# Performance work log

Hardware: AMD Instinct MI355X
Metric: run time of the kernel (lower is better)

## Reference

```python
import math
import jax, jax.numpy as jnp
import numpy as np


def _pairwise_sqdist(x, y):
    # x: [N, d], y: [M, d] -> [N, M]
    x2 = jnp.sum(x * x, axis=-1)[:, None]
    y2 = jnp.sum(y * y, axis=-1)[None, :]
    return jnp.maximum(x2 + y2 - 2.0 * (x @ y.T), 0.0)


def setup_inputs() -> dict:
    key = jax.random.key(0)
    k1, k2 = jax.random.split(key)
    N, M, D = 8192, 8192, 2
    base_points = jax.random.normal(k1, (N, D), dtype=jnp.float32)
    target_points = jax.random.normal(k2, (M, D), dtype=jnp.float32)
    log_sigma = jnp.asarray(math.log(0.1), dtype=jnp.float32)
    log_scale = jnp.zeros((D,), dtype=jnp.float32)
    return {
        "base_points": base_points,
        "target_points": target_points,
        "log_sigma": log_sigma,
        "log_scale": log_scale,
    }


def reference(base_points, target_points, log_sigma, log_scale):
    # learn_scale=True: anisotropic per-coordinate scaling
    scale = jnp.exp(log_scale)
    base = base_points * scale
    target = target_points * scale

    # uniform node weights (use_weight_net=False)
    N = base.shape[0]
    M = target.shape[0]
    w_base = jnp.full((N,), 1.0 / N, dtype=base.dtype)
    w_target = jnp.full((M,), 1.0 / M, dtype=target.dtype)

    # center=True: subtract weighted centroid of each cloud
    base = base - jnp.sum(w_base[:, None] * base, axis=0, keepdims=True)
    target = target - jnp.sum(w_target[:, None] * target, axis=0, keepdims=True)

    sigma = jnp.exp(log_sigma)
    inv2s2 = 1.0 / (2.0 * sigma * sigma)

    k_bb = jnp.exp(-_pairwise_sqdist(base, base) * inv2s2)      # [N, N]
    k_tt = jnp.exp(-_pairwise_sqdist(target, target) * inv2s2)  # [M, M]
    k_bt = jnp.exp(-_pairwise_sqdist(base, target) * inv2s2)    # [N, M]

    term_bb = w_base @ (k_bb @ w_base)
    term_tt = w_target @ (k_tt @ w_target)
    term_bt = w_base @ (k_bt @ w_target)
    loss = term_bb + term_tt - 2.0 * term_bt
    return loss
```

## Files before the change

### kernel.cpp

```cpp
#include <hip/hip_runtime.h>


#define BLOCK 256
#define NT_CROSS 1024
#define NT_TOT   2080
#define LOG2E  1.4426950408889634f
#define NBUCK  512
#define BXMIN  (-64.0f)
#define BSCALE 4.0f
#define CUT    6.32455532f

typedef float v2f __attribute__((ext_vector_type(2)));

struct Prep { float f0, f1, sh0, sh1; };

__device__ __forceinline__ float fexp2(float x) {
    return __builtin_amdgcn_exp2f(x);
}

__global__ __launch_bounds__(1024) void prep_kernel(
    const float* __restrict__ base, const float* __restrict__ target,
    const float* __restrict__ log_sigma, const float* __restrict__ log_scale,
    int N, int M, Prep* __restrict__ pp, double* __restrict__ slots)
{
    __shared__ double mred[16][4];
    const int tid = threadIdx.x;
    if (tid < 64) slots[tid] = 0.0;

    double sbx = 0, sby = 0, stx = 0, sty = 0;
    const float4* b4 = (const float4*)base;
    const float4* t4 = (const float4*)target;
    for (int i = tid; i < (N >> 1); i += 1024) {
        float4 v = b4[i];
        sbx += (double)v.x + (double)v.z;
        sby += (double)v.y + (double)v.w;
    }
    for (int i = tid; i < (M >> 1); i += 1024) {
        float4 v = t4[i];
        stx += (double)v.x + (double)v.z;
        sty += (double)v.y + (double)v.w;
    }
    for (int off = 32; off; off >>= 1) {
        sbx += __shfl_down(sbx, off); sby += __shfl_down(sby, off);
        stx += __shfl_down(stx, off); sty += __shfl_down(sty, off);
    }
    if ((tid & 63) == 0) {
        mred[tid >> 6][0] = sbx; mred[tid >> 6][1] = sby;
        mred[tid >> 6][2] = stx; mred[tid >> 6][3] = sty;
    }
    __syncthreads();
    if (tid == 0) {
        double b0 = 0, b1 = 0, t0 = 0, t1 = 0;
        for (int k = 0; k < 16; ++k) {
            b0 += mred[k][0]; b1 += mred[k][1];
            t0 += mred[k][2]; t1 += mred[k][3];
        }
        float s0 = expf(log_scale[0]);
        float s1 = expf(log_scale[1]);
        float sigma = expf(log_sigma[0]);
        float inv2s2 = 1.0f / (2.0f * sigma * sigma);
        float sq = sqrtf(inv2s2 * LOG2E);
        float f0 = s0 * sq, f1 = s1 * sq;
        pp->f0 = f0; pp->f1 = f1;
        pp->sh0 = (float)(b0 / (double)N - t0 / (double)M) * f0;
        pp->sh1 = (float)(b1 / (double)N - t1 / (double)M) * f1;
    }
}

__global__ __launch_bounds__(1024) void sort_kernel(
    const float* __restrict__ base, const float* __restrict__ target,
    int N, int M, const Prep* __restrict__ pp,
    float* __restrict__ xsB, float* __restrict__ ysB, float* __restrict__ csB,
    float* __restrict__ xsT, float* __restrict__ ysT, float* __restrict__ csT)
{
    __shared__ unsigned hist[NBUCK];
    __shared__ unsigned pref[NBUCK];
    __shared__ unsigned cnt[NBUCK];
    const int tid = threadIdx.x;
    const Prep p = *pp;
    const bool isB = (blockIdx.x == 0);
    const float2* src = (const float2*)(isB ? base : target);
    const int n = isB ? N : M;
    float* xs = isB ? xsB : xsT;
    float* ys = isB ? ysB : ysT;
    float* cs = isB ? csB : csT;
    const float shx = isB ? p.sh0 : 0.f;
    const float shy = isB ? p.sh1 : 0.f;

    for (int i = tid; i < NBUCK; i += 1024) { hist[i] = 0u; cnt[i] = 0u; }
    __syncthreads();
    for (int i = tid; i < n; i += 1024) {
        float2 a = src[i];
        float x = fmaf(a.x, p.f0, -shx);
        int b = (int)((x - BXMIN) * BSCALE);
        b = min(max(b, 0), NBUCK - 1);
        atomicAdd(&hist[b], 1u);
    }
    __syncthreads();
    if (tid < NBUCK) pref[tid] = hist[tid];
    __syncthreads();
    for (int off = 1; off < NBUCK; off <<= 1) {
        unsigned v = 0u;
        if (tid < NBUCK && tid >= off) v = pref[tid - off];
        __syncthreads();
        if (tid < NBUCK) pref[tid] += v;
        __syncthreads();
    }
    for (int i = tid; i < n; i += 1024) {
        float2 a = src[i];
        float x = fmaf(a.x, p.f0, -shx);
        float y = fmaf(a.y, p.f1, -shy);
        int b = (int)((x - BXMIN) * BSCALE);
        b = min(max(b, 0), NBUCK - 1);
        unsigned pos = pref[b] - hist[b] + atomicAdd(&cnt[b], 1u);
        xs[pos] = x;
        ys[pos] = y;
        cs[pos] = -fmaf(x, x, y * y);
    }
}

__global__ __launch_bounds__(BLOCK, 8) void mmd_main(
    int N, int M,
    const float* __restrict__ xsB, const float* __restrict__ ysB,
    const float* __restrict__ csB,
    const float* __restrict__ xsT, const float* __restrict__ ysT,
    const float* __restrict__ csT,
    double* __restrict__ slots)
{
    __shared__ __align__(16) float tbx[256];
    __shared__ __align__(16) float tby[256];
    __shared__ __align__(16) float tbc[256];
    __shared__ __align__(8)  float2 qb[64];
    __shared__ double wredd[4];

    const int tid = threadIdx.x;
    const int t   = (int)(((long long)blockIdx.x * 997) % NT_TOT);

    const double wNN = 1.0 / ((double)N * (double)N);
    const double wMM = 1.0 / ((double)M * (double)M);
    const double wNM = -2.0 / ((double)N * (double)M);

    int ib, jb, term;
    bool diag;
    const float* xA; const float* yA; const float* cA;
    const float* xB; const float* yB; const float* cB;
    double wt;
    if (t < NT_CROSS) {
        ib = t >> 5; jb = t & 31;
        xA = xsB; yA = ysB; cA = csB;
        xB = xsT; yB = ysT; cB = csT;
        wt = wNM; diag = false; term = 2;
    } else {
        const int u = t - NT_CROSS;
        term = (u >= 528) ? 1 : 0;
        const int v = u - term * 528;
        int r = (int)((65.0f - sqrtf(4225.0f - 8.0f * (float)v)) * 0.5f);
        r = min(max(r, 0), 31);
        while (r > 0 && (r * (65 - r)) / 2 > v) --r;
        while (r < 31 && ((r + 1) * (64 - r)) / 2 <= v) ++r;
        ib = r;
        jb = r + (v - (r * (65 - r)) / 2);
        diag = (jb == ib);
        if (term) { xA = xsT; yA = ysT; cA = csT; }
        else      { xA = xsB; yA = ysB; cA = csB; }
        xB = xA; yB = yA; cB = cA;
        wt = 2.0 * (term ? wMM : wNN);
    }
    const int i0 = ib * 256, j0 = jb * 256;

    tbx[tid] = xB[j0 + tid];
    tby[tid] = yB[j0 + tid];
    tbc[tid] = cB[j0 + tid];
    if (tid < 64) {
        float4 q4 = ((const float4*)(xB + j0))[tid];
        float qlo = fminf(fminf(q4.x, q4.y), fminf(q4.z, q4.w));
        float qhi = fmaxf(fmaxf(q4.x, q4.y), fmaxf(q4.z, q4.w));
        qb[tid] = make_float2(qlo, qhi);
    }
    __syncthreads();

    const int u_  = tid & 127;
    const int r0  = i0 + 2 * u_;
    const int js  = (tid >> 7) * 128;

    float2 xr = ((const float2*)xA)[r0 >> 1];
    float2 yr = ((const float2*)yA)[r0 >> 1];
    float2 cr = ((const float2*)cA)[r0 >> 1];
    float ax2s[2] = { xr.x + xr.x, xr.y + xr.y };
    float ay2s[2] = { yr.x + yr.x, yr.y + yr.y };
    float A0s[2]  = { cr.x, cr.y };

    float rmin = fminf(xr.x, xr.y);
    float rmax = fmaxf(xr.x, xr.y);
    for (int off = 32; off; off >>= 1) {
        rmin = fminf(rmin, __shfl_xor(rmin, off));
        rmax = fmaxf(rmax, __shfl_xor(rmax, off));
    }
    const float rminc = rmin - CUT;
    const float rmaxc = rmax + CUT;

    const float4* bx4 = (const float4*)(tbx + js);
    const float4* by4 = (const float4*)(tby + js);
    const float4* c4  = (const float4*)(tbc + js);
    const int qoff = js >> 2;

    double result;
    if (!diag) {
        v2f s00 = {0.f, 0.f}, s01 = {0.f, 0.f};
        v2f s10 = {0.f, 0.f}, s11 = {0.f, 0.f};
#pragma unroll 2
        for (int q = 0; q < 32; ++q) {
            float2 qr = qb[qoff + q];
            if (qr.x > rmaxc || qr.y < rminc) continue;
            float4 BX = bx4[q];
            float4 BY = by4[q];
            float4 C  = c4[q];
            v2f bxa = { BX.x, BX.y }, bxb = { BX.z, BX.w };
            v2f bya = { BY.x, BY.y }, byb = { BY.z, BY.w };
            v2f ca  = { C.x,  C.y  }, cb  = { C.z,  C.w  };
            {
                v2f A0v = { A0s[0], A0s[0] };
                v2f axv = { ax2s[0], ax2s[0] };
                v2f ayv = { ay2s[0], ay2s[0] };
                v2f ea = axv * bxa + (ayv * bya + (ca + A0v));
                v2f eb = axv * bxb + (ayv * byb + (cb + A0v));
                s00 += (v2f){ fexp2(ea.x), fexp2(ea.y) };
                s01 += (v2f){ fexp2(eb.x), fexp2(eb.y) };
            }
            {
                v2f A0v = { A0s[1], A0s[1] };
                v2f axv = { ax2s[1], ax2s[1] };
                v2f ayv = { ay2s[1], ay2s[1] };
                v2f ea = axv * bxa + (ayv * bya + (ca + A0v));
                v2f eb = axv * bxb + (ayv * byb + (cb + A0v));
                s10 += (v2f){ fexp2(ea.x), fexp2(ea.y) };
                s11 += (v2f){ fexp2(eb.x), fexp2(eb.y) };
            }
        }
        v2f st0 = s00 + s01;
        v2f st1 = s10 + s11;
        result = wt * ((double)(st0.x + st0.y) + (double)(st1.x + st1.y));
    } else {
        float sge = 0.f, sgt = 0.f;
        const int jbase = j0 + js;
#pragma unroll 2
        for (int q = 0; q < 32; ++q) {
            float2 qr = qb[qoff + q];
            if (qr.x > rmaxc || qr.y < rminc) continue;
            float4 BX = bx4[q];
            float4 BY = by4[q];
            float4 C  = c4[q];
            const int j = jbase + 4 * q;
#pragma unroll
            for (int k = 0; k < 2; ++k) {
                const int row = r0 + k;
                float e0 = fmaf(ax2s[k], BX.x, fmaf(ay2s[k], BY.x, C.x + A0s[k]));
                float e1 = fmaf(ax2s[k], BX.y, fmaf(ay2s[k], BY.y, C.y + A0s[k]));
                float e2 = fmaf(ax2s[k], BX.z, fmaf(ay2s[k], BY.z, C.z + A0s[k]));
                float e3 = fmaf(ax2s[k], BX.w, fmaf(ay2s[k], BY.w, C.w + A0s[k]));
                float v0 = fexp2(e0), v1 = fexp2(e1);
                float v2 = fexp2(e2), v3 = fexp2(e3);
                sge += (j + 0 >= row) ? v0 : 0.f;  sgt += (j + 0 > row) ? v0 : 0.f;
                sge += (j + 1 >= row) ? v1 : 0.f;  sgt += (j + 1 > row) ? v1 : 0.f;
                sge += (j + 2 >= row) ? v2 : 0.f;  sgt += (j + 2 > row) ? v2 : 0.f;
                sge += (j + 3 >= row) ? v3 : 0.f;  sgt += (j + 3 > row) ? v3 : 0.f;
            }
        }
        result = (term ? wMM : wNN) * (double)(sge + sgt);
    }

    for (int off = 32; off; off >>= 1) result += __shfl_down(result, off);
    if ((tid & 63) == 0) wredd[tid >> 6] = result;
    __syncthreads();
    if (tid == 0) {
        double s = wredd[0] + wredd[1] + wredd[2] + wredd[3];
        atomicAdd(&slots[blockIdx.x & 63], s);
    }
}

__global__ void final_kernel(const double* __restrict__ slots,
                             float* __restrict__ out)
{
    const int tid = threadIdx.x;
    double s = slots[tid];
    for (int off = 32; off; off >>= 1) s += __shfl_down(s, off);
    if (tid == 0) out[0] = (float)s;
}

extern "C" void kernel_launch(void* const* d_in, const int* in_sizes, int n_in,
                              void* d_out, int out_size, void* d_ws, size_t ws_size,
                              hipStream_t stream)
{
    const float* base      = (const float*)d_in[0];
    const float* target    = (const float*)d_in[1];
    const float* log_sigma = (const float*)d_in[2];
    const float* log_scale = (const float*)d_in[3];
    float* out = (float*)d_out;

    int N = in_sizes[0] / 2;
    int M = in_sizes[1] / 2;

    char* ws = (char*)d_ws;
    Prep*   pp    = (Prep*)ws;
    double* slots = (double*)(ws + 256);
    float*  arr   = (float*)(ws + 1024);
    float* xsB = arr;
    float* ysB = xsB + N;
    float* csB = ysB + N;
    float* xsT = csB + N;
    float* ysT = xsT + M;
    float* csT = ysT + M;

    prep_kernel<<<1, 1024, 0, stream>>>(base, target, log_sigma, log_scale,
                                        N, M, pp, slots);
    sort_kernel<<<2, 1024, 0, stream>>>(base, target, N, M, pp,
                                        xsB, ysB, csB, xsT, ysT, csT);
    mmd_main<<<NT_TOT, BLOCK, 0, stream>>>(N, M, xsB, ysB, csB,
                                           xsT, ysT, csT, slots);
    final_kernel<<<1, 64, 0, stream>>>(slots, out);
}
```

Baseline: 102.1 us.

## Fuse prep into sort and interleave column tiles for balanced MMD blocks

Removes the separate prep kernel. Each sort block now computes its own coordinate sums, and the base-minus-target centroid shift is applied per row inside the main kernel. Column tiles are now strided (phase-interleaved) rather than contiguous, so every block sees a spread of the sorted x-range, and the symmetric terms use full 32x32 grids with a per-block triangular mask instead of the upper-triangle enumeration. The cutoff radius is reduced. The goals are fewer launches and more even per-block work, at the cost of launching more blocks (3072) and losing some pruning locality from the interleaving.

```diff
diff --git a/kernel.cpp b/kernel.cpp
--- a/kernel.cpp
+++ b/kernel.cpp
@@ -1,102 +1,69 @@
 #include <hip/hip_runtime.h>
 
 
-#define BLOCK 256
+#define BLOCK    256
 #define NT_CROSS 1024
-#define NT_TOT   2080
-#define LOG2E  1.4426950408889634f
-#define NBUCK  512
-#define BXMIN  (-64.0f)
-#define BSCALE 4.0f
-#define CUT    6.32455532f
+#define NT_TOT   3072
+#define NBUCK    512
+#define BXMIN    (-64.0f)
+#define BSCALE   4.0f
+#define CUT      5.2915026f
+#define LOG2E    1.4426950408889634f
 
 typedef float v2f __attribute__((ext_vector_type(2)));
-
-struct Prep { float f0, f1, sh0, sh1; };
 
 __device__ __forceinline__ float fexp2(float x) {
     return __builtin_amdgcn_exp2f(x);
 }
 
-__global__ __launch_bounds__(1024) void prep_kernel(
+__global__ __launch_bounds__(1024) void sort_kernel(
     const float* __restrict__ base, const float* __restrict__ target,
     const float* __restrict__ log_sigma, const float* __restrict__ log_scale,
-    int N, int M, Prep* __restrict__ pp, double* __restrict__ slots)
+    int N, int M,
+    float* __restrict__ xsB, float* __restrict__ ysB, float* __restrict__ csB,
+    float* __restrict__ xsT, float* __restrict__ ysT, float* __restrict__ csT,
+    double* __restrict__ msum, double* __restrict__ slots)
 {
-    __shared__ double mred[16][4];
+    __shared__ unsigned hist[NBUCK], pref[NBUCK], cnt[NBUCK];
+    __shared__ double mred[16][2];
     const int tid = threadIdx.x;
-    if (tid < 64) slots[tid] = 0.0;
-
-    double sbx = 0, sby = 0, stx = 0, sty = 0;
-    const float4* b4 = (const float4*)base;
-    const float4* t4 = (const float4*)target;
-    for (int i = tid; i < (N >> 1); i += 1024) {
-        float4 v = b4[i];
-        sbx += (double)v.x + (double)v.z;
-        sby += (double)v.y + (double)v.w;
-    }
-    for (int i = tid; i < (M >> 1); i += 1024) {
-        float4 v = t4[i];
-        stx += (double)v.x + (double)v.z;
-        sty += (double)v.y + (double)v.w;
-    }
-    for (int off = 32; off; off >>= 1) {
-        sbx += __shfl_down(sbx, off); sby += __shfl_down(sby, off);
-        stx += __shfl_down(stx, off); sty += __shfl_down(sty, off);
-    }
-    if ((tid & 63) == 0) {
-        mred[tid >> 6][0] = sbx; mred[tid >> 6][1] = sby;
-        mred[tid >> 6][2] = stx; mred[tid >> 6][3] = sty;
-    }
-    __syncthreads();
-    if (tid == 0) {
-        double b0 = 0, b1 = 0, t0 = 0, t1 = 0;
-        for (int k = 0; k < 16; ++k) {
-            b0 += mred[k][0]; b1 += mred[k][1];
-            t0 += mred[k][2]; t1 += mred[k][3];
-        }
-        float s0 = expf(log_scale[0]);
-        float s1 = expf(log_scale[1]);
-        float sigma = expf(log_sigma[0]);
-        float inv2s2 = 1.0f / (2.0f * sigma * sigma);
-        float sq = sqrtf(inv2s2 * LOG2E);
-        float f0 = s0 * sq, f1 = s1 * sq;
-        pp->f0 = f0; pp->f1 = f1;
-        pp->sh0 = (float)(b0 / (double)N - t0 / (double)M) * f0;
-        pp->sh1 = (float)(b1 / (double)N - t1 / (double)M) * f1;
-    }
-}
-
-__global__ __launch_bounds__(1024) void sort_kernel(
-    const float* __restrict__ base, const float* __restrict__ target,
-    int N, int M, const Prep* __restrict__ pp,
-    float* __restrict__ xsB, float* __restrict__ ysB, float* __restrict__ csB,
-    float* __restrict__ xsT, float* __restrict__ ysT, float* __restrict__ csT)
-{
-    __shared__ unsigned hist[NBUCK];
-    __shared__ unsigned pref[NBUCK];
-    __shared__ unsigned cnt[NBUCK];
-    const int tid = threadIdx.x;
-    const Prep p = *pp;
     const bool isB = (blockIdx.x == 0);
+    if (isB && tid < 64) slots[tid] = 0.0;
+
+    const float sigma = expf(log_sigma[0]);
+    const float sq = sqrtf((0.5f / (sigma * sigma)) * LOG2E);
+    const float f0 = expf(log_scale[0]) * sq;
+    const float f1 = expf(log_scale[1]) * sq;
+
     const float2* src = (const float2*)(isB ? base : target);
     const int n = isB ? N : M;
     float* xs = isB ? xsB : xsT;
     float* ys = isB ? ysB : ysT;
     float* cs = isB ? csB : csT;
-    const float shx = isB ? p.sh0 : 0.f;
-    const float shy = isB ? p.sh1 : 0.f;
 
     for (int i = tid; i < NBUCK; i += 1024) { hist[i] = 0u; cnt[i] = 0u; }
     __syncthreads();
+
+    double sx = 0.0, sy = 0.0;
     for (int i = tid; i < n; i += 1024) {
         float2 a = src[i];
-        float x = fmaf(a.x, p.f0, -shx);
-        int b = (int)((x - BXMIN) * BSCALE);
-        b = min(max(b, 0), NBUCK - 1);
+        float x = a.x * f0, y = a.y * f1;
+        sx += (double)x; sy += (double)y;
+        int b = min(max((int)((x - BXMIN) * BSCALE), 0), NBUCK - 1);
         atomicAdd(&hist[b], 1u);
     }
-    __syncthreads();
+    for (int off = 32; off; off >>= 1) {
+        sx += __shfl_down(sx, off);
+        sy += __shfl_down(sy, off);
+    }
+    if ((tid & 63) == 0) { mred[tid >> 6][0] = sx; mred[tid >> 6][1] = sy; }
+    __syncthreads();
+    if (tid == 0) {
+        double ax = 0, ay = 0;
+        for (int k = 0; k < 16; ++k) { ax += mred[k][0]; ay += mred[k][1]; }
+        msum[2 * blockIdx.x] = ax; msum[2 * blockIdx.x + 1] = ay;
+    }
+
     if (tid < NBUCK) pref[tid] = hist[tid];
     __syncthreads();
     for (int off = 1; off < NBUCK; off <<= 1) {
@@ -108,10 +75,8 @@
     }
     for (int i = tid; i < n; i += 1024) {
         float2 a = src[i];
-        float x = fmaf(a.x, p.f0, -shx);
-        float y = fmaf(a.y, p.f1, -shy);
-        int b = (int)((x - BXMIN) * BSCALE);
-        b = min(max(b, 0), NBUCK - 1);
+        float x = a.x * f0, y = a.y * f1;
+        int b = min(max((int)((x - BXMIN) * BSCALE), 0), NBUCK - 1);
         unsigned pos = pref[b] - hist[b] + atomicAdd(&cnt[b], 1u);
         xs[pos] = x;
         ys[pos] = y;
@@ -125,7 +90,7 @@
     const float* __restrict__ csB,
     const float* __restrict__ xsT, const float* __restrict__ ysT,
     const float* __restrict__ csT,
-    double* __restrict__ slots)
+    const double* __restrict__ msum, double* __restrict__ slots)
 {
     __shared__ __align__(16) float tbx[256];
     __shared__ __align__(16) float tby[256];
@@ -134,87 +99,88 @@
     __shared__ double wredd[4];
 
     const int tid = threadIdx.x;
-    const int t   = (int)(((long long)blockIdx.x * 997) % NT_TOT);
+    const int t   = blockIdx.x;
 
     const double wNN = 1.0 / ((double)N * (double)N);
     const double wMM = 1.0 / ((double)M * (double)M);
     const double wNM = -2.0 / ((double)N * (double)M);
 
-    int ib, jb, term;
-    bool diag;
-    const float* xA; const float* yA; const float* cA;
-    const float* xB; const float* yB; const float* cB;
+    int rt, phase, term;
+    bool sym;
+    const float *xA, *yA, *xB, *yB, *cB;
     double wt;
+    float shx = 0.f, shy = 0.f;
     if (t < NT_CROSS) {
-        ib = t >> 5; jb = t & 31;
-        xA = xsB; yA = ysB; cA = csB;
-        xB = xsT; yB = ysT; cB = csT;
-        wt = wNM; diag = false; term = 2;
+        sym = false; term = 2;
+        rt = t >> 5; phase = t & 31;
+        xA = xsB; yA = ysB; xB = xsT; yB = ysT; cB = csT;
+        wt = wNM;
+        shx = (float)(msum[0] / (double)N - msum[2] / (double)M);
+        shy = (float)(msum[1] / (double)N - msum[3] / (double)M);
     } else {
+        sym = true;
         const int u = t - NT_CROSS;
-        term = (u >= 528) ? 1 : 0;
-        const int v = u - term * 528;
-        int r = (int)((65.0f - sqrtf(4225.0f - 8.0f * (float)v)) * 0.5f);
-        r = min(max(r, 0), 31);
-        while (r > 0 && (r * (65 - r)) / 2 > v) --r;
-        while (r < 31 && ((r + 1) * (64 - r)) / 2 <= v) ++r;
-        ib = r;
-        jb = r + (v - (r * (65 - r)) / 2);
-        diag = (jb == ib);
-        if (term) { xA = xsT; yA = ysT; cA = csT; }
-        else      { xA = xsB; yA = ysB; cA = csB; }
-        xB = xA; yB = yA; cB = cA;
+        term = (u >= 1024) ? 1 : 0;
+        const int v = u & 1023;
+        rt = v >> 5; phase = v & 31;
+        if (term) { xA = xsT; yA = ysT; xB = xsT; yB = ysT; cB = csT; }
+        else      { xA = xsB; yA = ysB; xB = xsB; yB = ysB; cB = csB; }
         wt = 2.0 * (term ? wMM : wNN);
     }
-    const int i0 = ib * 256, j0 = jb * 256;
-
-    tbx[tid] = xB[j0 + tid];
-    tby[tid] = yB[j0 + tid];
-    tbc[tid] = cB[j0 + tid];
-    if (tid < 64) {
-        float4 q4 = ((const float4*)(xB + j0))[tid];
-        float qlo = fminf(fminf(q4.x, q4.y), fminf(q4.z, q4.w));
-        float qhi = fmaxf(fmaxf(q4.x, q4.y), fmaxf(q4.z, q4.w));
-        qb[tid] = make_float2(qlo, qhi);
-    }
-    __syncthreads();
-
-    const int u_  = tid & 127;
-    const int r0  = i0 + 2 * u_;
-    const int js  = (tid >> 7) * 128;
-
-    float2 xr = ((const float2*)xA)[r0 >> 1];
-    float2 yr = ((const float2*)yA)[r0 >> 1];
-    float2 cr = ((const float2*)cA)[r0 >> 1];
-    float ax2s[2] = { xr.x + xr.x, xr.y + xr.y };
-    float ay2s[2] = { yr.x + yr.x, yr.y + yr.y };
-    float A0s[2]  = { cr.x, cr.y };
-
-    float rmin = fminf(xr.x, xr.y);
-    float rmax = fmaxf(xr.x, xr.y);
+    const int i0  = rt * 256;
+    const int jq0 = 4 * phase;
+
+    {
+        const int g = tid & 63;
+        const int addr = jq0 + 128 * g;
+        if (tid < 64) {
+            float4 v4 = *(const float4*)(xB + addr);
+            *(float4*)&tbx[4 * g] = v4;
+            qb[g] = make_float2(fminf(fminf(v4.x, v4.y), fminf(v4.z, v4.w)),
+                                fmaxf(fmaxf(v4.x, v4.y), fmaxf(v4.z, v4.w)));
+        } else if (tid < 128) {
+            *(float4*)&tby[4 * g] = *(const float4*)(yB + addr);
+        } else if (tid < 192) {
+            *(float4*)&tbc[4 * g] = *(const float4*)(cB + addr);
+        }
+    }
+    __syncthreads();
+
+    const int u_    = tid & 127;
+    const int r0    = i0 + 2 * u_;
+    const int qoff  = (tid >> 7) * 32;
+    const int wr_lo = i0 + ((tid >> 6) & 1) * 128;
+    const int wr_hi = wr_lo + 127;
+
+    float2 xr = *(const float2*)(xA + r0);
+    float2 yr = *(const float2*)(yA + r0);
+    const float axr0 = xr.x - shx, axr1 = xr.y - shx;
+    const float ayr0 = yr.x - shy, ayr1 = yr.y - shy;
+    const float ax2s[2] = { axr0 + axr0, axr1 + axr1 };
+    const float ay2s[2] = { ayr0 + ayr0, ayr1 + ayr1 };
+    const float A0s[2]  = { -fmaf(axr0, axr0, ayr0 * ayr0),
+                            -fmaf(axr1, axr1, ayr1 * ayr1) };
+
+    float rmin = fminf(axr0, axr1), rmax = fmaxf(axr0, axr1);
     for (int off = 32; off; off >>= 1) {
         rmin = fminf(rmin, __shfl_xor(rmin, off));
         rmax = fmaxf(rmax, __shfl_xor(rmax, off));
     }
-    const float rminc = rmin - CUT;
-    const float rmaxc = rmax + CUT;
-
-    const float4* bx4 = (const float4*)(tbx + js);
-    const float4* by4 = (const float4*)(tby + js);
-    const float4* c4  = (const float4*)(tbc + js);
-    const int qoff = js >> 2;
-
-    double result;
-    if (!diag) {
-        v2f s00 = {0.f, 0.f}, s01 = {0.f, 0.f};
-        v2f s10 = {0.f, 0.f}, s11 = {0.f, 0.f};
+    const float rminc = rmin - CUT, rmaxc = rmax + CUT;
+
+    v2f s00 = {0.f, 0.f}, s01 = {0.f, 0.f};
+    v2f s10 = {0.f, 0.f}, s11 = {0.f, 0.f};
+    float sge = 0.f, sgt = 0.f;
+
+    if (!sym) {
 #pragma unroll 2
-        for (int q = 0; q < 32; ++q) {
-            float2 qr = qb[qoff + q];
+        for (int m = 0; m < 32; ++m) {
+            const int qi = qoff + m;
+            float2 qr = qb[qi];
             if (qr.x > rmaxc || qr.y < rminc) continue;
-            float4 BX = bx4[q];
-            float4 BY = by4[q];
-            float4 C  = c4[q];
+            float4 BX = *(const float4*)&tbx[4 * qi];
+            float4 BY = *(const float4*)&tby[4 * qi];
+            float4 C  = *(const float4*)&tbc[4 * qi];
             v2f bxa = { BX.x, BX.y }, bxb = { BX.z, BX.w };
             v2f bya = { BY.x, BY.y }, byb = { BY.z, BY.w };
             v2f ca  = { C.x,  C.y  }, cb  = { C.z,  C.w  };
@@ -237,44 +203,69 @@
                 s11 += (v2f){ fexp2(eb.x), fexp2(eb.y) };
             }
         }
-        v2f st0 = s00 + s01;
-        v2f st1 = s10 + s11;
-        result = wt * ((double)(st0.x + st0.y) + (double)(st1.x + st1.y));
     } else {
-        float sge = 0.f, sgt = 0.f;
-        const int jbase = j0 + js;
 #pragma unroll 2
-        for (int q = 0; q < 32; ++q) {
-            float2 qr = qb[qoff + q];
-            if (qr.x > rmaxc || qr.y < rminc) continue;
-            float4 BX = bx4[q];
-            float4 BY = by4[q];
-            float4 C  = c4[q];
-            const int j = jbase + 4 * q;
+        for (int m = 0; m < 32; ++m) {
+            const int qi = qoff + m;
+            const int jq = jq0 + 128 * qi;
+            if (jq + 3 < wr_lo) continue;
+            const bool mask = (jq <= wr_hi);
+            float2 qr = qb[qi];
+            if (!mask && (qr.x > rmaxc || qr.y < rminc)) continue;
+            float4 BX = *(const float4*)&tbx[4 * qi];
+            float4 BY = *(const float4*)&tby[4 * qi];
+            float4 C  = *(const float4*)&tbc[4 * qi];
+            if (!mask) {
+                v2f bxa = { BX.x, BX.y }, bxb = { BX.z, BX.w };
+                v2f bya = { BY.x, BY.y }, byb = { BY.z, BY.w };
+                v2f ca  = { C.x,  C.y  }, cb  = { C.z,  C.w  };
+                {
+                    v2f A0v = { A0s[0], A0s[0] };
+                    v2f axv = { ax2s[0], ax2s[0] };
+                    v2f ayv = { ay2s[0], ay2s[0] };
+                    v2f ea = axv * bxa + (ayv * bya + (ca + A0v));
+                    v2f eb = axv * bxb + (ayv * byb + (cb + A0v));
+                    s00 += (v2f){ fexp2(ea.x), fexp2(ea.y) };
+                    s01 += (v2f){ fexp2(eb.x), fexp2(eb.y) };
+                }
+                {
+                    v2f A0v = { A0s[1], A0s[1] };
+                    v2f axv = { ax2s[1], ax2s[1] };
+                    v2f ayv = { ay2s[1], ay2s[1] };
+                    v2f ea = axv * bxa + (ayv * bya + (ca + A0v));
+                    v2f eb = axv * bxb + (ayv * byb + (cb + A0v));
+                    s10 += (v2f){ fexp2(ea.x), fexp2(ea.y) };
+                    s11 += (v2f){ fexp2(eb.x), fexp2(eb.y) };
+                }
+            } else {
 #pragma unroll
-            for (int k = 0; k < 2; ++k) {
-                const int row = r0 + k;
-                float e0 = fmaf(ax2s[k], BX.x, fmaf(ay2s[k], BY.x, C.x + A0s[k]));
-                float e1 = fmaf(ax2s[k], BX.y, fmaf(ay2s[k], BY.y, C.y + A0s[k]));
-                float e2 = fmaf(ax2s[k], BX.z, fmaf(ay2s[k], BY.z, C.z + A0s[k]));
-                float e3 = fmaf(ax2s[k], BX.w, fmaf(ay2s[k], BY.w, C.w + A0s[k]));
-                float v0 = fexp2(e0), v1 = fexp2(e1);
-                float v2 = fexp2(e2), v3 = fexp2(e3);
-                sge += (j + 0 >= row) ? v0 : 0.f;  sgt += (j + 0 > row) ? v0 : 0.f;
-                sge += (j + 1 >= row) ? v1 : 0.f;  sgt += (j + 1 > row) ? v1 : 0.f;
-                sge += (j + 2 >= row) ? v2 : 0.f;  sgt += (j + 2 > row) ? v2 : 0.f;
-                sge += (j + 3 >= row) ? v3 : 0.f;  sgt += (j + 3 > row) ? v3 : 0.f;
+                for (int k = 0; k < 2; ++k) {
+                    const int row = r0 + k;
+                    float e0 = fmaf(ax2s[k], BX.x, fmaf(ay2s[k], BY.x, C.x + A0s[k]));
+                    float e1 = fmaf(ax2s[k], BX.y, fmaf(ay2s[k], BY.y, C.y + A0s[k]));
+                    float e2 = fmaf(ax2s[k], BX.z, fmaf(ay2s[k], BY.z, C.z + A0s[k]));
+                    float e3 = fmaf(ax2s[k], BX.w, fmaf(ay2s[k], BY.w, C.w + A0s[k]));
+                    float v0 = fexp2(e0), v1 = fexp2(e1);
+                    float v2 = fexp2(e2), v3 = fexp2(e3);
+                    sge += (jq + 0 >= row) ? v0 : 0.f;  sgt += (jq + 0 > row) ? v0 : 0.f;
+                    sge += (jq + 1 >= row) ? v1 : 0.f;  sgt += (jq + 1 > row) ? v1 : 0.f;
+                    sge += (jq + 2 >= row) ? v2 : 0.f;  sgt += (jq + 2 > row) ? v2 : 0.f;
+                    sge += (jq + 3 >= row) ? v3 : 0.f;  sgt += (jq + 3 > row) ? v3 : 0.f;
+                }
             }
         }
-        result = (term ? wMM : wNN) * (double)(sge + sgt);
-    }
+    }
+
+    v2f st0 = s00 + s01, st1 = s10 + s11;
+    double result = wt * ((double)(st0.x + st0.y) + (double)(st1.x + st1.y));
+    if (sym) result += (term ? wMM : wNN) * (double)(sge + sgt);
 
     for (int off = 32; off; off >>= 1) result += __shfl_down(result, off);
     if ((tid & 63) == 0) wredd[tid >> 6] = result;
     __syncthreads();
     if (tid == 0) {
         double s = wredd[0] + wredd[1] + wredd[2] + wredd[3];
-        atomicAdd(&slots[blockIdx.x & 63], s);
+        atomicAdd(&slots[t & 63], s);
     }
 }
 
@@ -301,8 +292,8 @@
     int M = in_sizes[1] / 2;
 
     char* ws = (char*)d_ws;
-    Prep*   pp    = (Prep*)ws;
-    double* slots = (double*)(ws + 256);
+    double* msum  = (double*)ws;
+    double* slots = (double*)(ws + 64);
     float*  arr   = (float*)(ws + 1024);
     float* xsB = arr;
     float* ysB = xsB + N;
@@ -311,11 +302,10 @@
     float* ysT = xsT + M;
     float* csT = ysT + M;
 
-    prep_kernel<<<1, 1024, 0, stream>>>(base, target, log_sigma, log_scale,
-                                        N, M, pp, slots);
-    sort_kernel<<<2, 1024, 0, stream>>>(base, target, N, M, pp,
-                                        xsB, ysB, csB, xsT, ysT, csT);
+    sort_kernel<<<2, 1024, 0, stream>>>(base, target, log_sigma, log_scale,
+                                        N, M, xsB, ysB, csB, xsT, ysT, csT,
+                                        msum, slots);
     mmd_main<<<NT_TOT, BLOCK, 0, stream>>>(N, M, xsB, ysB, csB,
-                                           xsT, ysT, csT, slots);
+                                           xsT, ysT, csT, msum, slots);
     final_kernel<<<1, 64, 0, stream>>>(slots, out);
 }
```

Measured after the change: 98.92 us. 1.03x faster.
